# Kernel tuning notes

Measured on AMD Instinct MI355X. Metric: run time of the kernel, lower is better.

## Reference

```python
import jax, jax.numpy as jnp
import numpy as np

N = 2048      # global node count (num_global_nodes)
K = 8         # number of clients
NK = 1024     # local nodes per client
TAU_C = 0.5
GAMMA = 1.0
TAU_S = 0.5


def setup_inputs() -> dict:
    key = jax.random.key(0)
    k1, k2 = jax.random.split(key)
    # local adjacencies in [0,1) so thresholds tau_c/tau_s are meaningful
    client_adj = jax.random.uniform(k1, (K, NK, NK), dtype=jnp.float32)
    # per-client global node ids: sorted, duplicate-free subset of range(N)
    perm_keys = jax.random.split(k2, K)
    perms = jax.vmap(lambda k: jax.random.permutation(k, N)[:NK])(perm_keys)
    client_idx = jnp.sort(perms, axis=1).astype(jnp.int32)
    return {"client_adj": client_adj, "client_idx": client_idx}


def reference(client_adj, client_idx):
    # client_adj: [K, Nk, Nk] float, client_idx: [K, Nk] int
    Kc = client_adj.shape[0]
    dt = client_adj.dtype
    karr = jnp.arange(Kc)[:, None, None]           # [K,1,1]
    ix = client_idx[:, :, None]                    # [K,Nk,1] row ids (meshgrid 'ij')
    iy = client_idx[:, None, :]                    # [K,1,Nk] col ids

    # scatter each client's local adjacency into the common node space
    A_stack = jnp.zeros((Kc, N, N), dt).at[karr, ix, iy].set(client_adj)  # [K,N,N]
    mask = jnp.zeros((Kc, N, N), dt).at[karr, ix, iy].set(jnp.ones_like(client_adj))

    num_obs = jnp.maximum(mask.sum(axis=0), 1e-5)                 # [N,N]
    A_mean = (A_stack * mask).sum(axis=0) / num_obs               # consensus mean
    C = ((A_stack > TAU_C).astype(dt) * mask).sum(axis=0) / num_obs  # consensus rate
    V = (((A_stack - A_mean[None]) ** 2) * mask).sum(axis=0) / num_obs  # variance
    S = C * jnp.exp(-GAMMA * V)                                   # invariance score
    M_inv = (S > TAU_S).astype(dt)
    A_inv = M_inv * A_mean * (num_obs > 1e-5).astype(dt)
    return A_inv
```

## Files before the change

kernel.cpp:

```cpp
#include <hip/hip_runtime.h>
#include <math.h>

#define N  2048
#define K  8
#define NK 1024
#define R  4
#define TPB 512
#define SLOT NK
#define TAU_C 0.5f
#define TAU_S 0.5f

__global__ void __launch_bounds__(TPB, 4)
fia_fused(const float* __restrict__ adj,
          const int*   __restrict__ idx,
          float* __restrict__ out) {
    __shared__ short  jj[K][N];
    __shared__ short  ixs[K][R];
    __shared__ float  stage[K][NK + 4];
    __shared__ float  lutCS[81];
    __shared__ float2 lutB[81];

    const int tid = threadIdx.x;
    const int X0  = blockIdx.x * R;

    {
        int4  m1 = make_int4(-1, -1, -1, -1);
        int4* p4 = (int4*)&jj[0][0];
        #pragma unroll
        for (int q = 0; q < (K * N * 2) / (16 * TPB); ++q)
            p4[q * TPB + tid] = m1;
        if (tid < K * R) ((short*)ixs)[tid] = (short)-1;
        if (tid < K) stage[tid][SLOT] = 0.0f;
        if (tid < 81) {
            int cn = tid / 9, cc = tid % 9;
            float nn = fmaxf((float)cn, 1e-5f);
            float C  = (float)cc / nn;
            lutCS[tid] = C;
            float lo, hi;
            if (2 * cc <= cn) {
                lo = -2.0f; hi = -1.0f;
            } else {
                float B = logf(2.0f * C);
                float d = 1e-3f * (1.0f + fabsf(B));
                lo = (B - d) * (float)cn;
                hi = (B + d) * (float)cn;
            }
            lutB[tid] = make_float2(lo, hi);
        }
    }
    __syncthreads();

    #pragma unroll
    for (int it = 0; it < (K * NK) / (4 * TPB); ++it) {
        int  t4   = it * TPB + tid;
        int4 w    = ((const int4*)idx)[t4];
        int  base = t4 * 4;
        int  k    = base >> 10;
        int  p    = base & (NK - 1);
        jj[k][w.x] = (short)(p);
        jj[k][w.y] = (short)(p + 1);
        jj[k][w.z] = (short)(p + 2);
        jj[k][w.w] = (short)(p + 3);
        int r0 = w.x - X0, r1 = w.y - X0, r2 = w.z - X0, r3 = w.w - X0;
        if ((unsigned)r0 < (unsigned)R) ixs[k][r0] = (short)(p);
        if ((unsigned)r1 < (unsigned)R) ixs[k][r1] = (short)(p + 1);
        if ((unsigned)r2 < (unsigned)R) ixs[k][r2] = (short)(p + 2);
        if ((unsigned)r3 < (unsigned)R) ixs[k][r3] = (short)(p + 3);
    }
    __syncthreads();

    const int y0 = tid * 4;
    int jc[K][4];
    int jmask[4] = {0, 0, 0, 0};
    #pragma unroll
    for (int k = 0; k < K; ++k) {
        short4 v = *(const short4*)&jj[k][y0];
        int j0 = v.x, j1 = v.y, j2 = v.z, j3 = v.w;
        jmask[0] |= (j0 >= 0) ? (1 << k) : 0;
        jmask[1] |= (j1 >= 0) ? (1 << k) : 0;
        jmask[2] |= (j2 >= 0) ? (1 << k) : 0;
        jmask[3] |= (j3 >= 0) ? (1 << k) : 0;
        jc[k][0] = (j0 >= 0) ? j0 : SLOT;
        jc[k][1] = (j1 >= 0) ? j1 : SLOT;
        jc[k][2] = (j2 >= 0) ? j2 : SLOT;
        jc[k][3] = (j3 >= 0) ? j3 : SLOT;
    }

    #pragma unroll 1
    for (int r = 0; r < R; ++r) {
        int kp = 0;
        int ixr[K];
        #pragma unroll
        for (int k = 0; k < K; ++k) {
            int v = (int)ixs[k][r];
            ixr[k] = __builtin_amdgcn_readfirstlane(v);
            kp |= (ixr[k] >= 0) ? (1 << k) : 0;
        }

        float2 sr[K];
        #pragma unroll
        for (int k = 0; k < K; ++k) {
            if (ixr[k] >= 0) {
                const float2* __restrict__ src =
                    (const float2*)(adj + ((size_t)k * NK + (size_t)ixr[k]) * NK);
                sr[k] = src[tid];
            }
        }
        __syncthreads();
        #pragma unroll
        for (int k = 0; k < K; ++k) {
            if (ixr[k] >= 0)
                ((float2*)&stage[k][0])[tid] = sr[k];
        }
        __syncthreads();

        float vraw[4][K];
        float sum[4] = {0.f, 0.f, 0.f, 0.f};
        int   csi[4] = {0, 0, 0, 0};
        #pragma unroll
        for (int k = 0; k < K; ++k) {
            if ((kp >> k) & 1) {
                #pragma unroll
                for (int yy = 0; yy < 4; ++yy) {
                    float a = stage[k][jc[k][yy]];
                    vraw[yy][k] = a;
                    sum[yy] += a;
                    csi[yy] += (a > TAU_C) ? 1 : 0;
                }
            }
        }

        float res[4];
        #pragma unroll
        for (int yy = 0; yy < 4; ++yy) {
            const int m   = jmask[yy] & kp;
            const int cnt = __popc(m);
            float n    = fmaxf((float)cnt, 1e-5f);
            float mean = sum[yy] / n;

            float vs = 0.f;
            #pragma unroll
            for (int k = 0; k < K; ++k) {
                if ((kp >> k) & 1) {
                    bool  p = (m >> k) & 1;
                    float d = vraw[yy][k] - mean;
                    vs += p ? d * d : 0.f;
                }
            }

            const int li = cnt * 9 + csi[yy];
            float2 bb = lutB[li];
            bool acc;
            if (__builtin_expect(vs >= bb.x && vs <= bb.y, 0)) {
                float C = lutCS[li];
                float V = vs / n;
                float S = C * expf(-V);
                acc = (S > TAU_S);
            } else {
                acc = (vs < bb.x);
            }
            res[yy] = acc ? mean : 0.f;
        }

        float4 o;
        o.x = res[0]; o.y = res[1]; o.z = res[2]; o.w = res[3];
        *(float4*)(out + (size_t)(X0 + r) * N + y0) = o;
    }
}

extern "C" void kernel_launch(void* const* d_in, const int* in_sizes, int n_in,
                              void* d_out, int out_size, void* d_ws, size_t ws_size,
                              hipStream_t stream) {
    const float* adj = (const float*)d_in[0];
    const int*   idx = (const int*)d_in[1];
    float*       out = (float*)d_out;

    dim3 block(TPB, 1, 1);
    dim3 grid(N / R, 1, 1);
    fia_fused<<<grid, block, 0, stream>>>(adj, idx, out);
}
```

Before: 22.28 us.

## Double-buffer adjacency rows in LDS via async global-to-LDS loads

Replaces the register-staged row load with direct global_load_lds copies into a double-buffered LDS stage, prefetching the next row's client rows while the current row is computed. The stage buffers share LDS with the index map through a union, so the kernel's shared footprint stays roughly the same. This aims to hide global load latency and drop the register round-trip and one barrier per row. The cost is a full vmcnt(0) wait, which also waits on the output store, an extra barrier after the jc setup, and unused padding lanes in the copies.

```diff
diff --git a/kernel.cpp b/kernel.cpp
--- a/kernel.cpp
+++ b/kernel.cpp
@@ -10,36 +10,45 @@
 #define TAU_C 0.5f
 #define TAU_S 0.5f
 
+__device__ __forceinline__ void async_copy16(const float* g, float* l) {
+    __builtin_amdgcn_global_load_lds(
+        (__attribute__((address_space(1))) void*)(uintptr_t)(g),
+        (__attribute__((address_space(3))) void*)(uint32_t)(uintptr_t)(l),
+        16, 0, 0);
+}
+
 __global__ void __launch_bounds__(TPB, 4)
 fia_fused(const float* __restrict__ adj,
           const int*   __restrict__ idx,
           float* __restrict__ out) {
-    __shared__ short  jj[K][N];
+    __shared__ union {
+        short jj[K][N];
+        float st[2][K][NK + 4];
+    } u;
     __shared__ short  ixs[K][R];
-    __shared__ float  stage[K][NK + 4];
     __shared__ float  lutCS[81];
     __shared__ float2 lutB[81];
 
-    const int tid = threadIdx.x;
-    const int X0  = blockIdx.x * R;
+    const int tid  = threadIdx.x;
+    const int lane = tid & 63;
+    const int wid  = tid >> 6;
+    const int X0   = blockIdx.x * R;
 
     {
         int4  m1 = make_int4(-1, -1, -1, -1);
-        int4* p4 = (int4*)&jj[0][0];
+        int4* p4 = (int4*)&u.jj[0][0];
         #pragma unroll
         for (int q = 0; q < (K * N * 2) / (16 * TPB); ++q)
             p4[q * TPB + tid] = m1;
         if (tid < K * R) ((short*)ixs)[tid] = (short)-1;
-        if (tid < K) stage[tid][SLOT] = 0.0f;
         if (tid < 81) {
             int cn = tid / 9, cc = tid % 9;
             float nn = fmaxf((float)cn, 1e-5f);
             float C  = (float)cc / nn;
             lutCS[tid] = C;
             float lo, hi;
-            if (2 * cc <= cn) {
-                lo = -2.0f; hi = -1.0f;
-            } else {
+            if (2 * cc <= cn) { lo = -2.0f; hi = -1.0f; }
+            else {
                 float B = logf(2.0f * C);
                 float d = 1e-3f * (1.0f + fabsf(B));
                 lo = (B - d) * (float)cn;
@@ -57,10 +66,10 @@
         int  base = t4 * 4;
         int  k    = base >> 10;
         int  p    = base & (NK - 1);
-        jj[k][w.x] = (short)(p);
-        jj[k][w.y] = (short)(p + 1);
-        jj[k][w.z] = (short)(p + 2);
-        jj[k][w.w] = (short)(p + 3);
+        u.jj[k][w.x] = (short)(p);
+        u.jj[k][w.y] = (short)(p + 1);
+        u.jj[k][w.z] = (short)(p + 2);
+        u.jj[k][w.w] = (short)(p + 3);
         int r0 = w.x - X0, r1 = w.y - X0, r2 = w.z - X0, r3 = w.w - X0;
         if ((unsigned)r0 < (unsigned)R) ixs[k][r0] = (short)(p);
         if ((unsigned)r1 < (unsigned)R) ixs[k][r1] = (short)(p + 1);
@@ -74,7 +83,7 @@
     int jmask[4] = {0, 0, 0, 0};
     #pragma unroll
     for (int k = 0; k < K; ++k) {
-        short4 v = *(const short4*)&jj[k][y0];
+        short4 v = *(const short4*)&u.jj[k][y0];
         int j0 = v.x, j1 = v.y, j2 = v.z, j3 = v.w;
         jmask[0] |= (j0 >= 0) ? (1 << k) : 0;
         jmask[1] |= (j1 >= 0) ? (1 << k) : 0;
@@ -85,44 +94,84 @@
         jc[k][2] = (j2 >= 0) ? j2 : SLOT;
         jc[k][3] = (j3 >= 0) ? j3 : SLOT;
     }
+    __syncthreads();
+
+    if (tid < K)          u.st[0][tid][SLOT] = 0.0f;
+    else if (tid < 2 * K) u.st[1][tid - K][SLOT] = 0.0f;
+
+    {
+        int kp0 = 0, ix0[K];
+        #pragma unroll
+        for (int k = 0; k < K; ++k) {
+            int v = (int)ixs[k][0];
+            ix0[k] = __builtin_amdgcn_readfirstlane(v);
+            kp0 |= (ix0[k] >= 0) ? (1 << k) : 0;
+        }
+        int slot = 0;
+        #pragma unroll
+        for (int k = 0; k < K; ++k) {
+            if ((kp0 >> k) & 1) {
+                const float* rowg = adj + ((size_t)k * NK + (size_t)ix0[k]) * NK;
+                #pragma unroll
+                for (int q = 0; q < 4; ++q) {
+                    if ((slot & 7) == wid)
+                        async_copy16(rowg + q * 256 + lane * 4,
+                                     &u.st[0][k][q * 256]);
+                    ++slot;
+                }
+            }
+        }
+    }
+    asm volatile("s_waitcnt vmcnt(0)" ::: "memory");
+    __syncthreads();
 
     #pragma unroll 1
     for (int r = 0; r < R; ++r) {
-        int kp = 0;
-        int ixr[K];
-        #pragma unroll
-        for (int k = 0; k < K; ++k) {
-            int v = (int)ixs[k][r];
-            ixr[k] = __builtin_amdgcn_readfirstlane(v);
-            kp |= (ixr[k] >= 0) ? (1 << k) : 0;
-        }
-
-        float2 sr[K];
-        #pragma unroll
-        for (int k = 0; k < K; ++k) {
-            if (ixr[k] >= 0) {
-                const float2* __restrict__ src =
-                    (const float2*)(adj + ((size_t)k * NK + (size_t)ixr[k]) * NK);
-                sr[k] = src[tid];
-            }
-        }
-        __syncthreads();
-        #pragma unroll
-        for (int k = 0; k < K; ++k) {
-            if (ixr[k] >= 0)
-                ((float2*)&stage[k][0])[tid] = sr[k];
-        }
-        __syncthreads();
+        const int cur = r & 1;
+
+        int kpC = 0;
+        {
+            #pragma unroll
+            for (int k = 0; k < K; ++k) {
+                int v = (int)ixs[k][r];
+                kpC |= (__builtin_amdgcn_readfirstlane(v) >= 0) ? (1 << k) : 0;
+            }
+        }
+
+        if (r + 1 < R) {
+            const int nxt = cur ^ 1;
+            int kpN = 0, ixN[K];
+            #pragma unroll
+            for (int k = 0; k < K; ++k) {
+                int v = (int)ixs[k][r + 1];
+                ixN[k] = __builtin_amdgcn_readfirstlane(v);
+                kpN |= (ixN[k] >= 0) ? (1 << k) : 0;
+            }
+            int slot = 0;
+            #pragma unroll
+            for (int k = 0; k < K; ++k) {
+                if ((kpN >> k) & 1) {
+                    const float* rowg = adj + ((size_t)k * NK + (size_t)ixN[k]) * NK;
+                    #pragma unroll
+                    for (int q = 0; q < 4; ++q) {
+                        if ((slot & 7) == wid)
+                            async_copy16(rowg + q * 256 + lane * 4,
+                                         &u.st[nxt][k][q * 256]);
+                        ++slot;
+                    }
+                }
+            }
+        }
 
         float vraw[4][K];
         float sum[4] = {0.f, 0.f, 0.f, 0.f};
         int   csi[4] = {0, 0, 0, 0};
         #pragma unroll
         for (int k = 0; k < K; ++k) {
-            if ((kp >> k) & 1) {
+            if ((kpC >> k) & 1) {
                 #pragma unroll
                 for (int yy = 0; yy < 4; ++yy) {
-                    float a = stage[k][jc[k][yy]];
+                    float a = u.st[cur][k][jc[k][yy]];
                     vraw[yy][k] = a;
                     sum[yy] += a;
                     csi[yy] += (a > TAU_C) ? 1 : 0;
@@ -133,7 +182,7 @@
         float res[4];
         #pragma unroll
         for (int yy = 0; yy < 4; ++yy) {
-            const int m   = jmask[yy] & kp;
+            const int m   = jmask[yy] & kpC;
             const int cnt = __popc(m);
             float n    = fmaxf((float)cnt, 1e-5f);
             float mean = sum[yy] / n;
@@ -141,7 +190,7 @@
             float vs = 0.f;
             #pragma unroll
             for (int k = 0; k < K; ++k) {
-                if ((kp >> k) & 1) {
+                if ((kpC >> k) & 1) {
                     bool  p = (m >> k) & 1;
                     float d = vraw[yy][k] - mean;
                     vs += p ? d * d : 0.f;
@@ -165,6 +214,11 @@
         float4 o;
         o.x = res[0]; o.y = res[1]; o.z = res[2]; o.w = res[3];
         *(float4*)(out + (size_t)(X0 + r) * N + y0) = o;
+
+        if (r + 1 < R) {
+            asm volatile("s_waitcnt vmcnt(0)" ::: "memory");
+            __syncthreads();
+        }
     }
 }
 
```

Measured after the change: 26.76 us. 20.1% more time.
